# Optimization experiments

Hardware: AMD Instinct MI355X
Metric: run time of the kernel (lower is better)

The kernel has to match this reference:

```python
import jax, jax.numpy as jnp
import numpy as np


def _chamfer_one(x, y):
    # x: [N,3], y: [M,3]; squared-Euclidean pairwise distances via norm expansion
    x2 = jnp.sum(x * x, axis=-1)  # [N]
    y2 = jnp.sum(y * y, axis=-1)  # [M]
    cross = jnp.einsum('nd,md->nm', x, y)  # [N,M]
    d = x2[:, None] + y2[None, :] - 2.0 * cross  # [N,M] squared distances
    # kaolin chamfer_distance: mean of NN sq-dists in both directions, summed (w1=w2=1)
    return jnp.mean(jnp.min(d, axis=1)) + jnp.mean(jnp.min(d, axis=0))


def reference(x, y):
    # x, y: [B, N, 3] / [B, M, 3]
    per_sample = jax.vmap(_chamfer_one)(x, y)  # [B]
    return jnp.mean(per_sample)


def setup_inputs() -> dict:
    key = jax.random.key(0)
    kx, ky = jax.random.split(key)
    x = jax.random.normal(kx, (16, 4096, 3), dtype=jnp.float32)
    y = jax.random.normal(ky, (16, 4096, 3), dtype=jnp.float32)
    return {"x": x, "y": y}
```

## Files before the change

### kernel.cpp

```cpp
#include <hip/hip_runtime.h>
#include <hip/hip_fp16.h>
#include <math.h>


typedef _Float16 f16x8  __attribute__((ext_vector_type(8)));
typedef float    f32x16 __attribute__((ext_vector_type(16)));

constexpr int BATCH  = 16;
constexpr int NPTS   = 4096;
constexpr int NDB    = 2 * BATCH;
constexpr int BLOCK  = 512;
constexpr int QPB    = 256;
constexpr int CHUNK  = 512;
constexpr int NCHUNK = NPTS / CHUNK;
constexpr int NBLK   = NDB * (NPTS / QPB);

__device__ __forceinline__ void cvt_point(float a, float b, float c,
                                          _Float16& ha, _Float16& hb,
                                          _Float16& hc, _Float16& shi,
                                          _Float16& slo) {
    ha = (_Float16)a; hb = (_Float16)b; hc = (_Float16)c;
    float fa = (float)ha, fb = (float)hb, fc = (float)hc;
    float ss = fa * fa + fb * fb + fc * fc;
    shi = (_Float16)ss;
    slo = (_Float16)(ss - (float)shi);
}

__global__ void __launch_bounds__(BLOCK, 4)
chamfer_fused(const float* __restrict__ x, const float* __restrict__ y,
              float* __restrict__ partial) {
    const int bid   = blockIdx.x;
    const int qgrp  = bid & 15;
    const int db    = bid >> 4;
    const int dir   = db >> 4;
    const int batch = db & (BATCH - 1);
    const int lane  = threadIdx.x & 63;
    const int wave  = threadIdx.x >> 6;
    const int m     = lane & 31;

    const float* P  = dir ? y : x;
    const float* G  = dir ? x : y;
    const float* Pb = P + (size_t)batch * NPTS * 3;
    const float* Gb = G + (size_t)batch * NPTS * 3;

    const _Float16 one = (_Float16)1.0f, zz = (_Float16)0.0f;

    f16x8 bfrag;
    {
        int qi = qgrp * QPB + wave * 32 + m;
        _Float16 ha, hb, hc, shi, slo;
        cvt_point(Pb[3 * qi], Pb[3 * qi + 1], Pb[3 * qi + 2],
                  ha, hb, hc, shi, slo);
        bfrag = (f16x8){ ha, hb, hc, one, one, shi, slo, zz };
    }

    __shared__ f16x8 As[2][CHUNK];

    {
        int j = threadIdx.x;
        _Float16 ha, hb, hc, shi, slo;
        cvt_point(Gb[3 * j], Gb[3 * j + 1], Gb[3 * j + 2],
                  ha, hb, hc, shi, slo);
        As[0][threadIdx.x] = (f16x8){ (_Float16)(-2.0f * (float)ha),
                                      (_Float16)(-2.0f * (float)hb),
                                      (_Float16)(-2.0f * (float)hc),
                                      shi, slo, one, one, zz };
    }

    const f32x16 z = {0.0f, 0.0f, 0.0f, 0.0f, 0.0f, 0.0f, 0.0f, 0.0f,
                      0.0f, 0.0f, 0.0f, 0.0f, 0.0f, 0.0f, 0.0f, 0.0f};
    float acc0 = INFINITY, acc1 = INFINITY;

    for (int ch = 0; ch < NCHUNK; ++ch) {
        __syncthreads();
        const int cur = ch & 1;
        if (ch + 1 < NCHUNK) {
            int j = (ch + 1) * CHUNK + threadIdx.x;
            _Float16 ha, hb, hc, shi, slo;
            cvt_point(Gb[3 * j], Gb[3 * j + 1], Gb[3 * j + 2],
                      ha, hb, hc, shi, slo);
            As[cur ^ 1][threadIdx.x] = (f16x8){ (_Float16)(-2.0f * (float)ha),
                                                (_Float16)(-2.0f * (float)hb),
                                                (_Float16)(-2.0f * (float)hc),
                                                shi, slo, one, one, zz };
        }
        #pragma unroll 4
        for (int tt = 0; tt < CHUNK / 32; ++tt) {
            f16x8 af = As[cur][tt * 32 + m];
            f32x16 d = __builtin_amdgcn_mfma_f32_32x32x16_f16(af, bfrag, z,
                                                              0, 0, 0);
            acc0 = fminf(fminf(d[0],  d[1]),  acc0);
            acc1 = fminf(fminf(d[8],  d[9]),  acc1);
            acc0 = fminf(fminf(d[2],  d[3]),  acc0);
            acc1 = fminf(fminf(d[10], d[11]), acc1);
            acc0 = fminf(fminf(d[4],  d[5]),  acc0);
            acc1 = fminf(fminf(d[12], d[13]), acc1);
            acc0 = fminf(fminf(d[6],  d[7]),  acc0);
            acc1 = fminf(fminf(d[14], d[15]), acc1);
        }
    }
    float acc = fminf(acc0, acc1);

    acc = fminf(acc, __shfl_xor(acc, 32, 64));
    #pragma unroll
    for (int off = 1; off < 64; off <<= 1) acc += __shfl_xor(acc, off, 64);

    __shared__ float s8[8];
    if (lane == 0) s8[wave] = acc;
    __syncthreads();
    if (threadIdx.x == 0) {
        float b = ((s8[0] + s8[1]) + (s8[2] + s8[3])) +
                  ((s8[4] + s8[5]) + (s8[6] + s8[7]));
        partial[bid] = b;
    }
}

__global__ void __launch_bounds__(256)
finalize(const float* __restrict__ partial, float* __restrict__ out) {
    float s = partial[threadIdx.x] + partial[threadIdx.x + 256];
    #pragma unroll
    for (int off = 32; off > 0; off >>= 1) s += __shfl_down(s, off, 64);
    __shared__ float ws_s[4];
    if ((threadIdx.x & 63) == 0) ws_s[threadIdx.x >> 6] = s;
    __syncthreads();
    if (threadIdx.x == 0) {
        float b = (ws_s[0] + ws_s[1]) + (ws_s[2] + ws_s[3]);
        out[0] = b * (0.25f / ((float)BATCH * (float)NPTS));
    }
}

extern "C" void kernel_launch(void* const* d_in, const int* in_sizes, int n_in,
                              void* d_out, int out_size, void* d_ws, size_t ws_size,
                              hipStream_t stream) {
    const float* x = (const float*)d_in[0];
    const float* y = (const float*)d_in[1];
    float* out = (float*)d_out;
    float* partial = (float*)d_ws;

    hipLaunchKernelGGL(chamfer_fused, dim3(NBLK), dim3(BLOCK), 0, stream,
                       x, y, partial);
    hipLaunchKernelGGL(finalize, dim3(1), dim3(256), 0, stream, partial, out);
}
```

Baseline: 73.42 us.

## Give each wave two query tiles sharing one LDS A-fragment read

Halves the block to 4 waves and has each wave handle two 32-query tiles, issuing two MFMAs per LDS A-fragment load. This cuts LDS read traffic per MFMA and gives more independent MFMA work per wave to hide latency. CHUNK is doubled to 1024 so fewer barriers occur per block, each thread builds two fragments per chunk, and the min-reduction epilogue is updated for the two tiles. The cost is more registers (launch bounds drop to 2), more LDS per block, and fewer waves per block.

```diff
diff --git a/kernel.cpp b/kernel.cpp
--- a/kernel.cpp
+++ b/kernel.cpp
@@ -9,9 +9,9 @@
 constexpr int BATCH  = 16;
 constexpr int NPTS   = 4096;
 constexpr int NDB    = 2 * BATCH;
-constexpr int BLOCK  = 512;
+constexpr int BLOCK  = 256;
 constexpr int QPB    = 256;
-constexpr int CHUNK  = 512;
+constexpr int CHUNK  = 1024;
 constexpr int NCHUNK = NPTS / CHUNK;
 constexpr int NBLK   = NDB * (NPTS / QPB);
 
@@ -26,7 +26,18 @@
     slo = (_Float16)(ss - (float)shi);
 }
 
-__global__ void __launch_bounds__(BLOCK, 4)
+__device__ __forceinline__ f16x8 make_afrag(const float* __restrict__ Gb,
+                                            int j) {
+    const _Float16 one = (_Float16)1.0f, zz = (_Float16)0.0f;
+    _Float16 ha, hb, hc, shi, slo;
+    cvt_point(Gb[3 * j], Gb[3 * j + 1], Gb[3 * j + 2], ha, hb, hc, shi, slo);
+    return (f16x8){ (_Float16)(-2.0f * (float)ha),
+                    (_Float16)(-2.0f * (float)hb),
+                    (_Float16)(-2.0f * (float)hc),
+                    shi, slo, one, one, zz };
+}
+
+__global__ void __launch_bounds__(BLOCK, 2)
 chamfer_fused(const float* __restrict__ x, const float* __restrict__ y,
               float* __restrict__ partial) {
     const int bid   = blockIdx.x;
@@ -45,74 +56,79 @@
 
     const _Float16 one = (_Float16)1.0f, zz = (_Float16)0.0f;
 
-    f16x8 bfrag;
+    f16x8 bfrag0, bfrag1;
     {
-        int qi = qgrp * QPB + wave * 32 + m;
+        int qi0 = qgrp * QPB + (wave * 2 + 0) * 32 + m;
+        int qi1 = qgrp * QPB + (wave * 2 + 1) * 32 + m;
         _Float16 ha, hb, hc, shi, slo;
-        cvt_point(Pb[3 * qi], Pb[3 * qi + 1], Pb[3 * qi + 2],
+        cvt_point(Pb[3 * qi0], Pb[3 * qi0 + 1], Pb[3 * qi0 + 2],
                   ha, hb, hc, shi, slo);
-        bfrag = (f16x8){ ha, hb, hc, one, one, shi, slo, zz };
+        bfrag0 = (f16x8){ ha, hb, hc, one, one, shi, slo, zz };
+        cvt_point(Pb[3 * qi1], Pb[3 * qi1 + 1], Pb[3 * qi1 + 2],
+                  ha, hb, hc, shi, slo);
+        bfrag1 = (f16x8){ ha, hb, hc, one, one, shi, slo, zz };
     }
 
     __shared__ f16x8 As[2][CHUNK];
 
-    {
-        int j = threadIdx.x;
-        _Float16 ha, hb, hc, shi, slo;
-        cvt_point(Gb[3 * j], Gb[3 * j + 1], Gb[3 * j + 2],
-                  ha, hb, hc, shi, slo);
-        As[0][threadIdx.x] = (f16x8){ (_Float16)(-2.0f * (float)ha),
-                                      (_Float16)(-2.0f * (float)hb),
-                                      (_Float16)(-2.0f * (float)hc),
-                                      shi, slo, one, one, zz };
-    }
+    #pragma unroll
+    for (int r = 0; r < CHUNK / BLOCK; ++r)
+        As[0][r * BLOCK + threadIdx.x] = make_afrag(Gb, r * BLOCK + threadIdx.x);
 
     const f32x16 z = {0.0f, 0.0f, 0.0f, 0.0f, 0.0f, 0.0f, 0.0f, 0.0f,
                       0.0f, 0.0f, 0.0f, 0.0f, 0.0f, 0.0f, 0.0f, 0.0f};
-    float acc0 = INFINITY, acc1 = INFINITY;
+    float a00 = INFINITY, a01 = INFINITY;
+    float a10 = INFINITY, a11 = INFINITY;
 
     for (int ch = 0; ch < NCHUNK; ++ch) {
         __syncthreads();
         const int cur = ch & 1;
         if (ch + 1 < NCHUNK) {
-            int j = (ch + 1) * CHUNK + threadIdx.x;
-            _Float16 ha, hb, hc, shi, slo;
-            cvt_point(Gb[3 * j], Gb[3 * j + 1], Gb[3 * j + 2],
-                      ha, hb, hc, shi, slo);
-            As[cur ^ 1][threadIdx.x] = (f16x8){ (_Float16)(-2.0f * (float)ha),
-                                                (_Float16)(-2.0f * (float)hb),
-                                                (_Float16)(-2.0f * (float)hc),
-                                                shi, slo, one, one, zz };
+            #pragma unroll
+            for (int r = 0; r < CHUNK / BLOCK; ++r) {
+                int s = r * BLOCK + threadIdx.x;
+                As[cur ^ 1][s] = make_afrag(Gb, (ch + 1) * CHUNK + s);
+            }
         }
         #pragma unroll 4
         for (int tt = 0; tt < CHUNK / 32; ++tt) {
             f16x8 af = As[cur][tt * 32 + m];
-            f32x16 d = __builtin_amdgcn_mfma_f32_32x32x16_f16(af, bfrag, z,
-                                                              0, 0, 0);
-            acc0 = fminf(fminf(d[0],  d[1]),  acc0);
-            acc1 = fminf(fminf(d[8],  d[9]),  acc1);
-            acc0 = fminf(fminf(d[2],  d[3]),  acc0);
-            acc1 = fminf(fminf(d[10], d[11]), acc1);
-            acc0 = fminf(fminf(d[4],  d[5]),  acc0);
-            acc1 = fminf(fminf(d[12], d[13]), acc1);
-            acc0 = fminf(fminf(d[6],  d[7]),  acc0);
-            acc1 = fminf(fminf(d[14], d[15]), acc1);
+            f32x16 d0 = __builtin_amdgcn_mfma_f32_32x32x16_f16(af, bfrag0, z,
+                                                               0, 0, 0);
+            f32x16 d1 = __builtin_amdgcn_mfma_f32_32x32x16_f16(af, bfrag1, z,
+                                                               0, 0, 0);
+            a00 = fminf(fminf(d0[0],  d0[1]),  a00);
+            a01 = fminf(fminf(d0[8],  d0[9]),  a01);
+            a10 = fminf(fminf(d1[0],  d1[1]),  a10);
+            a11 = fminf(fminf(d1[8],  d1[9]),  a11);
+            a00 = fminf(fminf(d0[2],  d0[3]),  a00);
+            a01 = fminf(fminf(d0[10], d0[11]), a01);
+            a10 = fminf(fminf(d1[2],  d1[3]),  a10);
+            a11 = fminf(fminf(d1[10], d1[11]), a11);
+            a00 = fminf(fminf(d0[4],  d0[5]),  a00);
+            a01 = fminf(fminf(d0[12], d0[13]), a01);
+            a10 = fminf(fminf(d1[4],  d1[5]),  a10);
+            a11 = fminf(fminf(d1[12], d1[13]), a11);
+            a00 = fminf(fminf(d0[6],  d0[7]),  a00);
+            a01 = fminf(fminf(d0[14], d0[15]), a01);
+            a10 = fminf(fminf(d1[6],  d1[7]),  a10);
+            a11 = fminf(fminf(d1[14], d1[15]), a11);
         }
     }
-    float acc = fminf(acc0, acc1);
+    float acc0 = fminf(a00, a01);
+    float acc1 = fminf(a10, a11);
 
-    acc = fminf(acc, __shfl_xor(acc, 32, 64));
+    acc0 = fminf(acc0, __shfl_xor(acc0, 32, 64));
+    acc1 = fminf(acc1, __shfl_xor(acc1, 32, 64));
+    float acc = acc0 + acc1;
     #pragma unroll
     for (int off = 1; off < 64; off <<= 1) acc += __shfl_xor(acc, off, 64);
 
-    __shared__ float s8[8];
-    if (lane == 0) s8[wave] = acc;
+    __shared__ float s4[4];
+    if (lane == 0) s4[wave] = acc;
     __syncthreads();
-    if (threadIdx.x == 0) {
-        float b = ((s8[0] + s8[1]) + (s8[2] + s8[3])) +
-                  ((s8[4] + s8[5]) + (s8[6] + s8[7]));
-        partial[bid] = b;
-    }
+    if (threadIdx.x == 0)
+        partial[bid] = (s4[0] + s4[1]) + (s4[2] + s4[3]);
 }
 
 __global__ void __launch_bounds__(256)
```

Result: no change. 73.10 us (-0.4%).
